# Performance work log

Measured on AMD Instinct MI355X. Metric: run time of the kernel, lower is better.

## Reference

```python
import jax, jax.numpy as jnp
import numpy as np

N = 10000
E = 320000
IN_DIM = 256
HID = 128
HEADS = 3
NEG_SLOPE = 0.2
EPS = 1e-8


def setup_inputs() -> dict:
    key = jax.random.key(0)
    ks = jax.random.split(key, 12)
    rn = lambda k, s, sc=0.1: jax.random.normal(k, s, dtype=jnp.float32) * sc
    return {
        'x1': jax.random.normal(ks[0], (N, IN_DIM), dtype=jnp.float32),
        'edge_index1': jax.random.randint(ks[1], (2, E), 0, N, dtype=jnp.int64),
        'x2': jax.random.normal(ks[2], (N, IN_DIM), dtype=jnp.float32),
        'edge_index2': jax.random.randint(ks[3], (2, E), 0, N, dtype=jnp.int64),
        'W1': rn(ks[4], (IN_DIM, HEADS * HID)),
        'att_src1': rn(ks[5], (HEADS, HID)),
        'att_dst1': rn(ks[6], (HEADS, HID)),
        'b1': rn(ks[7], (HEADS * HID,)),
        'W2': rn(ks[8], (HEADS * HID, HID)),
        'att_src2': rn(ks[9], (1, HID)),
        'att_dst2': rn(ks[10], (1, HID)),
        'b2': rn(ks[11], (HID,)),
    }


def gat_conv(x, edge_index, W, a_src, a_dst, bias, heads, out_ch, concat):
    """PyG-style GATConv with add_self_loops=True."""
    n = x.shape[0]
    loops = jnp.arange(n, dtype=edge_index.dtype)
    ei = jnp.concatenate([edge_index, jnp.stack([loops, loops])], axis=1)
    src, dst = ei[0], ei[1]
    h = (x @ W).reshape(n, heads, out_ch)                    # [N,H,C]
    s = jnp.einsum('nhc,hc->nh', h, a_src)                    # alpha_src per node
    d = jnp.einsum('nhc,hc->nh', h, a_dst)                    # alpha_dst per node
    e = jax.nn.leaky_relu(s[src] + d[dst], NEG_SLOPE)         # [Etot,H]
    m = jax.ops.segment_max(e, dst, num_segments=n)           # segment softmax (stable)
    ex = jnp.exp(e - m[dst])
    denom = jax.ops.segment_sum(ex, dst, num_segments=n)
    alpha = ex / denom[dst]                                   # [Etot,H]
    out = jax.ops.segment_sum(h[src] * alpha[:, :, None], dst, num_segments=n)
    out = out.reshape(n, heads * out_ch) if concat else out.mean(axis=1)
    return out + bias, (ei, alpha)


def _branch(x, ei, W1, as1, ad1, b1, W2, as2, ad2, b2):
    e1, (ei_sl, alpha1) = gat_conv(x, ei, W1, as1, ad1, b1, HEADS, HID, True)
    e1 = jax.nn.relu(e1)
    e2, _ = gat_conv(e1, ei, W2, as2, ad2, b2, 1, HID, False)
    # _graph_pooling
    attn_val = alpha1.mean(axis=1)                            # [Etot]
    node_attn = jax.ops.segment_sum(attn_val, ei_sl[1], num_segments=x.shape[0])
    weighted = e2 * node_attn[:, None]
    pooled = jnp.concatenate([weighted.mean(axis=0), e2.mean(axis=0)])  # [2*HID]
    return pooled, alpha1


def reference(x1, edge_index1, x2, edge_index2, W1, att_src1, att_dst1, b1,
              W2, att_src2, att_dst2, b2):
    g1, alpha1 = _branch(x1, edge_index1, W1, att_src1, att_dst1, b1,
                         W2, att_src2, att_dst2, b2)
    g2, alpha2 = _branch(x2, edge_index2, W1, att_src1, att_dst1, b1,
                         W2, att_src2, att_dst2, b2)
    n1 = jnp.maximum(jnp.linalg.norm(g1), EPS)
    n2 = jnp.maximum(jnp.linalg.norm(g2), EPS)
    sim = jnp.dot(g1, g2) / (n1 * n2)
    return sim, alpha1, alpha2
```

## Files before the change

### kernel.cpp

```cpp
#include <hip/hip_runtime.h>
#include <hip/hip_bf16.h>
#include <cstdint>
#include <cstddef>

#define INDIM 256
#define NEG 0.2f

typedef __attribute__((ext_vector_type(8))) short short8v;
typedef __attribute__((ext_vector_type(4))) float f32x4;
typedef __attribute__((ext_vector_type(2))) float f32x2;

__device__ __forceinline__ unsigned short f2bf(float x) {
  __hip_bfloat16 b = __float2bfloat16(x);
  return __builtin_bit_cast(unsigned short, b);
}

__device__ __forceinline__ unsigned char f2fp8(float v) {
  int packed = __builtin_amdgcn_cvt_pk_fp8_f32(v, v, 0, false);
  return (unsigned char)(packed & 0xff);
}

__device__ __forceinline__ float lrelu(float v) { return v > 0.f ? v : NEG * v; }

__global__ void wprep_kernel(const float* __restrict__ W1, __hip_bfloat16* __restrict__ W1t,
                             const float* __restrict__ W2, __hip_bfloat16* __restrict__ W2t,
                             const float* __restrict__ x1, const float* __restrict__ x2,
                             unsigned short* __restrict__ xb, int N) {
  int idx = blockIdx.x * blockDim.x + threadIdx.x;
  const int T1 = 256 * 384;
  const int T2 = 384 * 128;
  if (idx < T1) {
    int k = idx / 384, c = idx - k * 384;
    W1t[(size_t)c * 256 + k] = __float2bfloat16(W1[idx]);
  } else if (idx < T1 + T2) {
    int i = idx - T1;
    int k = i / 128, c = i - k * 128;
    W2t[(size_t)c * 384 + k] = __float2bfloat16(W2[i]);
  } else {
    int j = idx - T1 - T2;
    if (j < 2 * N * 64) {
      int row = j >> 6, q = j & 63;
      const float* src = (row < N) ? (x1 + (size_t)row * 256) : (x2 + (size_t)(row - N) * 256);
      float4 v = *reinterpret_cast<const float4*>(src + 4 * q);
      uint2 st;
      st.x = (unsigned int)f2bf(v.x) | ((unsigned int)f2bf(v.y) << 16);
      st.y = (unsigned int)f2bf(v.z) | ((unsigned int)f2bf(v.w) << 16);
      *reinterpret_cast<uint2*>(xb + (size_t)row * 256 + 4 * q) = st;
    }
  }
}

template<int K, int SST>
__device__ __forceinline__ void gemm_body(int bx, int by,
                                          const short* __restrict__ Ab,
                                          const __hip_bfloat16* __restrict__ Wt,
                                          const float* __restrict__ att_s,
                                          const float* __restrict__ att_d,
                                          unsigned char* __restrict__ Yc,
                                          float* __restrict__ So,
                                          float* __restrict__ Do,
                                          int M, int NC,
                                          short (*As)[40], short (*Bs)[40],
                                          float (*sred)[64]) {
  const int tid = threadIdx.x;
  const int row0 = bx * 64;
  const int col0 = by * 128;
  const int l = tid & 63, w = tid >> 6;
  const int wr = w >> 1, wc = w & 1;
  const int lr = l & 15, lk = (l >> 4) * 8;

  f32x4 acc[2][4];
#pragma unroll
  for (int m = 0; m < 2; ++m)
#pragma unroll
    for (int n = 0; n < 4; ++n) acc[m][n] = {0.f, 0.f, 0.f, 0.f};

  for (int k0 = 0; k0 < K; k0 += 32) {
    __syncthreads();
    {
      int r = tid >> 2, kq = (tid & 3) * 8;
      int gr = row0 + r;
      short8v av = {0, 0, 0, 0, 0, 0, 0, 0};
      if (gr < M) av = *(const short8v*)(Ab + (size_t)gr * K + k0 + kq);
      *(short8v*)&As[r][kq] = av;
    }
    {
      int c = tid >> 1, kq = (tid & 1) * 8;
      const short* wp = (const short*)Wt + (size_t)(col0 + c) * K + k0 + kq;
      *(short8v*)&Bs[c][kq]      = *(const short8v*)wp;
      *(short8v*)&Bs[c][kq + 16] = *(const short8v*)(wp + 16);
    }
    __syncthreads();
    short8v a[2], b[4];
#pragma unroll
    for (int m = 0; m < 2; ++m) a[m] = *(short8v*)&As[wr * 32 + m * 16 + lr][lk];
#pragma unroll
    for (int n = 0; n < 4; ++n) b[n] = *(short8v*)&Bs[wc * 64 + n * 16 + lr][lk];
#pragma unroll
    for (int m = 0; m < 2; ++m)
#pragma unroll
      for (int n = 0; n < 4; ++n)
        acc[m][n] = __builtin_amdgcn_mfma_f32_16x16x32_bf16(a[m], b[n], acc[m][n], 0, 0, 0);
  }
#pragma unroll
  for (int m = 0; m < 2; ++m) {
    int rbase = row0 + wr * 32 + m * 16 + (l >> 4) * 4;
#pragma unroll
    for (int n = 0; n < 4; ++n) {
      int col = col0 + wc * 64 + n * 16 + lr;
#pragma unroll
      for (int q = 0; q < 4; ++q) {
        int row = rbase + q;
        if (row < M) Yc[(size_t)row * NC + col] = f2fp8(acc[m][n][q]);
      }
    }
  }
  float asv[4], adv[4];
#pragma unroll
  for (int n = 0; n < 4; ++n) {
    int col = col0 + wc * 64 + n * 16 + lr;
    asv[n] = att_s[col];
    adv[n] = att_d[col];
  }
  float ps[2][4], pd[2][4];
#pragma unroll
  for (int m = 0; m < 2; ++m)
#pragma unroll
    for (int q = 0; q < 4; ++q) {
      float s = 0.f, d = 0.f;
#pragma unroll
      for (int n = 0; n < 4; ++n) {
        s = fmaf(acc[m][n][q], asv[n], s);
        d = fmaf(acc[m][n][q], adv[n], d);
      }
      ps[m][q] = s; pd[m][q] = d;
    }
#pragma unroll
  for (int o = 1; o < 16; o <<= 1) {
#pragma unroll
    for (int m = 0; m < 2; ++m)
#pragma unroll
      for (int q = 0; q < 4; ++q) {
        ps[m][q] += __shfl_xor(ps[m][q], o);
        pd[m][q] += __shfl_xor(pd[m][q], o);
      }
  }
  __syncthreads();
  if (wc == 1 && lr == 0) {
#pragma unroll
    for (int m = 0; m < 2; ++m)
#pragma unroll
      for (int q = 0; q < 4; ++q) {
        int rl = wr * 32 + m * 16 + (l >> 4) * 4 + q;
        sred[0][rl] = ps[m][q];
        sred[1][rl] = pd[m][q];
      }
  }
  __syncthreads();
  if (wc == 0 && lr == 0) {
#pragma unroll
    for (int m = 0; m < 2; ++m)
#pragma unroll
      for (int q = 0; q < 4; ++q) {
        int rl = wr * 32 + m * 16 + (l >> 4) * 4 + q;
        int row = row0 + rl;
        if (row < M) {
          So[(size_t)row * SST + by] = ps[m][q] + sred[0][rl];
          Do[(size_t)row * SST + by] = pd[m][q] + sred[1][rl];
        }
      }
  }
}

__global__ __launch_bounds__(256) void gemm1_deg_kernel(const short* __restrict__ xb,
                                                        const __hip_bfloat16* __restrict__ Wt,
                                                        const float* __restrict__ att_s,
                                                        const float* __restrict__ att_d,
                                                        unsigned char* __restrict__ Yc,
                                                        float* __restrict__ So,
                                                        float* __restrict__ Do,
                                                        int M, int gmx,
                                                        const int* __restrict__ ed1,
                                                        const int* __restrict__ ed2,
                                                        int E, int Etot, int N,
                                                        int* __restrict__ deg) {
  __shared__ short As[64][40];
  __shared__ short Bs[128][40];
  __shared__ float sred[2][64];
  int bid = blockIdx.x;
  if (bid < gmx * 3) {
    gemm_body<256, 4>(bid % gmx, bid / gmx, xb, Wt, att_s, att_d,
                      Yc, So, Do, M, 384, As, Bs, sred);
  } else {
    int idx = (bid - gmx * 3) * 256 + threadIdx.x;
    if (idx < 2 * Etot) {
      int br = idx >= Etot;
      int el = idx - br * Etot;
      const int* ed = br ? ed2 : ed1;
      int dn = ((el < E) ? ed[el] : (el - E)) + br * N;
      atomicAdd(&deg[dn], 1);
    }
  }
}

__global__ __launch_bounds__(256) void gemm2_alpha_kernel(const short* __restrict__ e1b,
                                                          const __hip_bfloat16* __restrict__ Wt,
                                                          const float* __restrict__ att_s,
                                                          const float* __restrict__ att_d,
                                                          unsigned char* __restrict__ Yc,
                                                          float* __restrict__ So,
                                                          float* __restrict__ Do,
                                                          int M, int gmx,
                                                          const float* __restrict__ S4,
                                                          const float* __restrict__ D4,
                                                          const float* __restrict__ invden,
                                                          const int* __restrict__ es1,
                                                          const int* __restrict__ ed1,
                                                          const int* __restrict__ es2,
                                                          const int* __restrict__ ed2,
                                                          int E, int Etot, int N,
                                                          float* __restrict__ out) {
  __shared__ short As[64][40];
  __shared__ short Bs[128][40];
  __shared__ float sred[2][64];
  int bid = blockIdx.x;
  if (bid < gmx) {
    gemm_body<384, 1>(bid, 0, e1b, Wt, att_s, att_d,
                      Yc, So, Do, M, 128, As, Bs, sred);
  } else {
    int idx = (bid - gmx) * 256 + threadIdx.x;
    if (idx < 2 * Etot) {
      int br = idx >= Etot;
      int el = idx - br * Etot;
      const int* es = br ? es2 : es1;
      const int* ed = br ? ed2 : ed1;
      int sn, dn;
      if (el < E) { sn = es[el]; dn = ed[el]; } else { sn = dn = el - E; }
      sn += br * N; dn += br * N;
      float* ao = out + 1 + (size_t)br * Etot * 3 + (size_t)el * 3;
#pragma unroll
      for (int h = 0; h < 3; ++h) {
        float v = lrelu(S4[sn * 4 + h] + D4[dn * 4 + h]);
        ao[h] = __expf(v) * invden[dn * 3 + h];
      }
    }
  }
}

__global__ __launch_bounds__(1024) void scan_kernel(const int* __restrict__ deg,
                                                    int* __restrict__ rowptr,
                                                    int* __restrict__ cursor, int n) {
  __shared__ int wsum[16];
  int t = threadIdx.x, lane = t & 63, wid = t >> 6;
  int start = t * 20;
  int v[20];
  int s = 0;
#pragma unroll
  for (int k = 0; k < 20; ++k) {
    int i = start + k;
    int d = (i < n) ? deg[i] : 0;
    s += d;
    v[k] = s;
  }
  int x = s;
#pragma unroll
  for (int o = 1; o < 64; o <<= 1) {
    int tm = __shfl_up(x, o);
    if (lane >= o) x += tm;
  }
  if (lane == 63) wsum[wid] = x;
  __syncthreads();
  if (wid == 0) {
    int wv = (lane < 16) ? wsum[lane] : 0;
#pragma unroll
    for (int o = 1; o < 16; o <<= 1) {
      int tm = __shfl_up(wv, o);
      if (lane >= o) wv += tm;
    }
    if (lane < 16) wsum[lane] = wv;
  }
  __syncthreads();
  int excl = (x - s) + (wid ? wsum[wid - 1] : 0);
  if (t == 0) rowptr[0] = 0;
#pragma unroll
  for (int k = 0; k < 20; ++k) {
    int i = start + k;
    if (i < n) {
      rowptr[i + 1] = excl + v[k];
      cursor[i] = excl + (k ? v[k - 1] : 0);
    }
  }
}

__global__ void fill_kernel(const int* __restrict__ es1, const int* __restrict__ ed1,
                            const int* __restrict__ es2, const int* __restrict__ ed2,
                            int E, int Etot, int N, int* __restrict__ cursor,
                            int* __restrict__ csr_src) {
  int idx = blockIdx.x * blockDim.x + threadIdx.x;
  if (idx >= 2 * Etot) return;
  int br = idx >= Etot;
  int el = idx - br * Etot;
  const int* es = br ? es2 : es1;
  const int* ed = br ? ed2 : ed1;
  int sn, dn;
  if (el < E) { sn = es[el]; dn = ed[el]; } else { sn = dn = el - E; }
  sn += br * N; dn += br * N;
  int pos = atomicAdd(&cursor[dn], 1);
  csr_src[pos] = sn;
}

__global__ __launch_bounds__(256) void agg1_kernel(const unsigned char* __restrict__ h1c,
                                                   const float* __restrict__ S4,
                                                   const float* __restrict__ D4,
                                                   const int* __restrict__ rowptr,
                                                   const int* __restrict__ csr_src,
                                                   const float* __restrict__ b1,
                                                   __hip_bfloat16* __restrict__ e1b,
                                                   float* __restrict__ invden, int N2) {
  __shared__ float4 st[4][64];
  int wv = threadIdx.x >> 6;
  int n = blockIdx.x * 4 + wv;
  if (n >= N2) return;
  int l = threadIdx.x & 63;
  int head = l >> 5;
  const float4* S4v = reinterpret_cast<const float4*>(S4);
  int p0 = rowptr[n], p1 = rowptr[n + 1];
  float d0 = D4[n * 4], d1 = D4[n * 4 + 1], d2 = D4[n * 4 + 2];

  float dp0 = 0.f, dp1 = 0.f, dp2 = 0.f;
  float acc[6] = {0.f, 0.f, 0.f, 0.f, 0.f, 0.f};
  for (int base = p0; base < p1; base += 64) {
    int cnt = min(64, p1 - base);
    if (l < cnt) {
      int sn = csr_src[base + l];
      float4 sv = S4v[sn];
      float e0 = __expf(lrelu(sv.x + d0));
      float e1 = __expf(lrelu(sv.y + d1));
      float e2 = __expf(lrelu(sv.z + d2));
      st[wv][l] = make_float4(__int_as_float(sn), e0, e1, e2);
      dp0 += e0; dp1 += e1; dp2 += e2;
    }
    int i = 0;
    for (; i + 4 <= cnt; i += 4) {
      float4 w[4];
      unsigned int hv[4];
      unsigned short gv[4];
#pragma unroll
      for (int u = 0; u < 4; ++u) {
        w[u] = st[wv][i + u];
        int sn = __float_as_int(w[u].x);
        const unsigned char* row = h1c + (size_t)sn * 384;
        hv[u] = *reinterpret_cast<const unsigned int*>(row + 4 * l);
        gv[u] = *reinterpret_cast<const unsigned short*>(row + 256 + 2 * l);
      }
#pragma unroll
      for (int u = 0; u < 4; ++u) {
        float alo = head ? w[u].z : w[u].y;
        float ahi = w[u].w;
        f32x2 f0 = __builtin_amdgcn_cvt_pk_f32_fp8((int)hv[u], false);
        f32x2 f1 = __builtin_amdgcn_cvt_pk_f32_fp8((int)hv[u], true);
        f32x2 g0 = __builtin_amdgcn_cvt_pk_f32_fp8((int)(unsigned int)gv[u], false);
        acc[0] = fmaf(alo, f0.x, acc[0]);
        acc[1] = fmaf(alo, f0.y, acc[1]);
        acc[2] = fmaf(alo, f1.x, acc[2]);
        acc[3] = fmaf(alo, f1.y, acc[3]);
        acc[4] = fmaf(ahi, g0.x, acc[4]);
        acc[5] = fmaf(ahi, g0.y, acc[5]);
      }
    }
    for (; i < cnt; ++i) {
      float4 w = st[wv][i];
      int sn = __float_as_int(w.x);
      const unsigned char* row = h1c + (size_t)sn * 384;
      unsigned int hv = *reinterpret_cast<const unsigned int*>(row + 4 * l);
      unsigned short gv = *reinterpret_cast<const unsigned short*>(row + 256 + 2 * l);
      float alo = head ? w.z : w.y;
      float ahi = w.w;
      f32x2 f0 = __builtin_amdgcn_cvt_pk_f32_fp8((int)hv, false);
      f32x2 f1 = __builtin_amdgcn_cvt_pk_f32_fp8((int)hv, true);
      f32x2 g0 = __builtin_amdgcn_cvt_pk_f32_fp8((int)(unsigned int)gv, false);
      acc[0] = fmaf(alo, f0.x, acc[0]);
      acc[1] = fmaf(alo, f0.y, acc[1]);
      acc[2] = fmaf(alo, f1.x, acc[2]);
      acc[3] = fmaf(alo, f1.y, acc[3]);
      acc[4] = fmaf(ahi, g0.x, acc[4]);
      acc[5] = fmaf(ahi, g0.y, acc[5]);
    }
  }
#pragma unroll
  for (int o = 32; o; o >>= 1) {
    dp0 += __shfl_down(dp0, o); dp1 += __shfl_down(dp1, o); dp2 += __shfl_down(dp2, o);
  }
  float inv0 = 1.f / __shfl(dp0, 0);
  float inv1 = 1.f / __shfl(dp1, 0);
  float inv2 = 1.f / __shfl(dp2, 0);

  float ilo = head ? inv1 : inv0;
  int c0 = 4 * l;
  float4 bb = *reinterpret_cast<const float4*>(b1 + c0);
  float v0 = acc[0] * ilo + bb.x;
  float v1 = acc[1] * ilo + bb.y;
  float v2 = acc[2] * ilo + bb.z;
  float v3 = acc[3] * ilo + bb.w;
  v0 = v0 > 0.f ? v0 : 0.f; v1 = v1 > 0.f ? v1 : 0.f;
  v2 = v2 > 0.f ? v2 : 0.f; v3 = v3 > 0.f ? v3 : 0.f;
  int ch = 256 + 2 * l;
  float2 bh = *reinterpret_cast<const float2*>(b1 + ch);
  float v4 = acc[4] * inv2 + bh.x;
  float v5 = acc[5] * inv2 + bh.y;
  v4 = v4 > 0.f ? v4 : 0.f; v5 = v5 > 0.f ? v5 : 0.f;
  unsigned short* eb = reinterpret_cast<unsigned short*>(e1b) + (size_t)n * 384;
  uint2 lo;
  lo.x = (unsigned int)f2bf(v0) | ((unsigned int)f2bf(v1) << 16);
  lo.y = (unsigned int)f2bf(v2) | ((unsigned int)f2bf(v3) << 16);
  *reinterpret_cast<uint2*>(eb + c0) = lo;
  *reinterpret_cast<unsigned int*>(eb + ch) =
      (unsigned int)f2bf(v4) | ((unsigned int)f2bf(v5) << 16);
  if (l == 0) invden[n * 3] = inv0;
  else if (l == 1) invden[n * 3 + 1] = inv1;
  else if (l == 2) invden[n * 3 + 2] = inv2;
}

__global__ __launch_bounds__(256) void agg2_kernel(const unsigned char* __restrict__ h2c,
                                                   const float* __restrict__ S2,
                                                   const float* __restrict__ D2,
                                                   const int* __restrict__ rowptr,
                                                   const int* __restrict__ csr_src,
                                                   const float* __restrict__ b2,
                                                   float* __restrict__ e2out, int N2) {
  __shared__ int lsrc[4][256];
  __shared__ float la[4][256];
  const unsigned int* H4 = reinterpret_cast<const unsigned int*>(h2c);
  int wv = threadIdx.x >> 6;
  int n = blockIdx.x * 4 + wv;
  if (n >= N2) return;
  int lane = threadIdx.x & 63;
  int half = lane >> 5, t = lane & 31;
  int p0 = rowptr[n], p1 = rowptr[n + 1];
  float dnv = D2[n];

  float dpart = 0.f;
  float acc[4] = {0.f, 0.f, 0.f, 0.f};
  for (int base = p0; base < p1; base += 256) {
    int cnt = min(256, p1 - base);
    for (int i = lane; i < cnt; i += 64) {
      int sn = csr_src[base + i];
      lsrc[wv][i] = sn;
      float ex = __expf(lrelu(S2[sn] + dnv));
      la[wv][i] = ex;
      dpart += ex;
    }
    int i = half;
    for (; i + 14 < cnt; i += 16) {
      unsigned int hv[8];
      float av[8];
#pragma unroll
      for (int u = 0; u < 8; ++u) {
        int e = i + 2 * u;
        int sn = lsrc[wv][e];
        av[u] = la[wv][e];
        hv[u] = H4[(size_t)sn * 32 + t];
      }
#pragma unroll
      for (int u = 0; u < 8; ++u) {
        f32x2 f0 = __builtin_amdgcn_cvt_pk_f32_fp8((int)hv[u], false);
        f32x2 f1 = __builtin_amdgcn_cvt_pk_f32_fp8((int)hv[u], true);
        acc[0] = fmaf(av[u], f0.x, acc[0]);
        acc[1] = fmaf(av[u], f0.y, acc[1]);
        acc[2] = fmaf(av[u], f1.x, acc[2]);
        acc[3] = fmaf(av[u], f1.y, acc[3]);
      }
    }
    for (; i < cnt; i += 2) {
      int sn = lsrc[wv][i];
      float a = la[wv][i];
      unsigned int hv = H4[(size_t)sn * 32 + t];
      f32x2 f0 = __builtin_amdgcn_cvt_pk_f32_fp8((int)hv, false);
      f32x2 f1 = __builtin_amdgcn_cvt_pk_f32_fp8((int)hv, true);
      acc[0] = fmaf(a, f0.x, acc[0]);
      acc[1] = fmaf(a, f0.y, acc[1]);
      acc[2] = fmaf(a, f1.x, acc[2]);
      acc[3] = fmaf(a, f1.y, acc[3]);
    }
  }
#pragma unroll
  for (int k = 0; k < 4; ++k) acc[k] += __shfl_xor(acc[k], 32);
#pragma unroll
  for (int o = 32; o; o >>= 1) dpart += __shfl_down(dpart, o);
  float invden = 1.f / __shfl(dpart, 0);
  if (half == 0) {
    float4 bb = *reinterpret_cast<const float4*>(b2 + 4 * t);
    float4 ov;
    ov.x = acc[0] * invden + bb.x;
    ov.y = acc[1] * invden + bb.y;
    ov.z = acc[2] * invden + bb.z;
    ov.w = acc[3] * invden + bb.w;
    *reinterpret_cast<float4*>(e2out + (size_t)n * 128 + 4 * t) = ov;
  }
}

__global__ __launch_bounds__(128) void pool_sim_kernel(const float* __restrict__ e2,
                                                       float* __restrict__ g,
                                                       int* __restrict__ cnt,
                                                       int N, float invN,
                                                       float* __restrict__ out) {
  int c = threadIdx.x;
  int br = blockIdx.y;
  int r0 = br * N + blockIdx.x * 128;
  int r1 = min(r0 + 128, br * N + N);
  float acc = 0.f;
  for (int n = r0; n < r1; ++n) acc += e2[(size_t)n * 128 + c];
  atomicAdd(&g[br * 128 + c], acc * invN);
  __threadfence();
  __shared__ bool last;
  __shared__ float sd[128], s1[128], s2[128];
  if (c == 0) {
    int total = gridDim.x * gridDim.y;
    last = (atomicAdd(cnt, 1) == total - 1);
  }
  __syncthreads();
  if (!last) return;
  float a = atomicAdd(&g[c], 0.f);
  float b = atomicAdd(&g[128 + c], 0.f);
  sd[c] = a * b; s1[c] = a * a; s2[c] = b * b;
  __syncthreads();
  for (int ofs = 64; ofs; ofs >>= 1) {
    if (c < ofs) { sd[c] += sd[c + ofs]; s1[c] += s1[c + ofs]; s2[c] += s2[c + ofs]; }
    __syncthreads();
  }
  if (c == 0) {
    float n1 = fmaxf(sqrtf(s1[0]), 1e-8f);
    float n2 = fmaxf(sqrtf(s2[0]), 1e-8f);
    out[0] = sd[0] / (n1 * n2);
  }
}

extern "C" void kernel_launch(void* const* d_in, const int* in_sizes, int n_in,
                              void* d_out, int out_size, void* d_ws, size_t ws_size,
                              hipStream_t stream) {
  const int N = in_sizes[0] / INDIM;
  const int E = in_sizes[1] / 2;
  const int Etot = E + N;
  const int N2 = 2 * N;

  const float* x1  = (const float*)d_in[0];
  const int*   ei1 = (const int*)d_in[1];
  const float* x2  = (const float*)d_in[2];
  const int*   ei2 = (const int*)d_in[3];
  const float* W1  = (const float*)d_in[4];
  const float* as1 = (const float*)d_in[5];
  const float* ad1 = (const float*)d_in[6];
  const float* b1  = (const float*)d_in[7];
  const float* W2  = (const float*)d_in[8];
  const float* as2 = (const float*)d_in[9];
  const float* ad2 = (const float*)d_in[10];
  const float* b2  = (const float*)d_in[11];
  float* out = (float*)d_out;
  const int* es1 = ei1, *ed1 = ei1 + E;
  const int* es2 = ei2, *ed2 = ei2 + E;

  char* p = (char*)d_ws;
  auto alloc = [&](size_t bytes) -> char* {
    char* q = p;
    p += (bytes + 255) & ~(size_t)255;
    return q;
  };
  float* g   = (float*)alloc(256 * 4);
  int*   cnt = (int*)alloc(256);
  int*   deg = (int*)alloc((size_t)N2 * 4);
  size_t zero_bytes = (size_t)((char*)deg - (char*)g) + (((size_t)N2 * 4 + 255) & ~(size_t)255);

  unsigned short* xb = (unsigned short*)alloc((size_t)N2 * 256 * 2);
  unsigned char* h1c = (unsigned char*)alloc((size_t)N2 * 384);
  __hip_bfloat16* e1b = (__hip_bfloat16*)alloc((size_t)N2 * 384 * 2);
  unsigned char* h2c = (unsigned char*)alloc((size_t)N2 * 128);
  float* e2          = (float*)alloc((size_t)N2 * 128 * 4);
  __hip_bfloat16* W1t = (__hip_bfloat16*)alloc((size_t)256 * 384 * 2);
  __hip_bfloat16* W2t = (__hip_bfloat16*)alloc((size_t)384 * 128 * 2);
  float* s1v  = (float*)alloc((size_t)N2 * 4 * 4);
  float* d1v  = (float*)alloc((size_t)N2 * 4 * 4);
  float* s2v  = (float*)alloc((size_t)N2 * 4);
  float* d2v  = (float*)alloc((size_t)N2 * 4);
  float* idn  = (float*)alloc((size_t)N2 * 3 * 4);
  int* rowptr  = (int*)alloc((size_t)(N2 + 1) * 4);
  int* cursor  = (int*)alloc((size_t)N2 * 4);
  int* csr_src = (int*)alloc((size_t)2 * Etot * 4);

  const int EB = 256;
  const int egrid2 = (2 * Etot + EB - 1) / EB;
  const int gmx = (N2 + 63) / 64;
  const int wtot = 256 * 384 + 384 * 128 + N2 * 64;

  hipMemsetAsync(g, 0, zero_bytes, stream);
  wprep_kernel<<<(wtot + 255) / 256, 256, 0, stream>>>(W1, W1t, W2, W2t, x1, x2, xb, N);

  gemm1_deg_kernel<<<gmx * 3 + egrid2, 256, 0, stream>>>((const short*)xb, W1t, as1, ad1,
                                                         h1c, s1v, d1v, N2, gmx,
                                                         ed1, ed2, E, Etot, N, deg);
  scan_kernel<<<1, 1024, 0, stream>>>(deg, rowptr, cursor, N2);
  fill_kernel<<<egrid2, EB, 0, stream>>>(es1, ed1, es2, ed2, E, Etot, N, cursor, csr_src);

  agg1_kernel<<<(N2 + 3) / 4, 256, 0, stream>>>(h1c, s1v, d1v, rowptr, csr_src, b1,
                                                e1b, idn, N2);

  gemm2_alpha_kernel<<<gmx + egrid2, 256, 0, stream>>>((const short*)e1b, W2t, as2, ad2,
                                                       h2c, s2v, d2v, N2, gmx,
                                                       s1v, d1v, idn,
                                                       es1, ed1, es2, ed2, E, Etot, N, out);
  agg2_kernel<<<(N2 + 3) / 4, 256, 0, stream>>>(h2c, s2v, d2v, rowptr, csr_src, b2, e2, N2);

  pool_sim_kernel<<<dim3((N + 127) / 128, 2), 128, 0, stream>>>(e2, g, cnt, N,
                                                                1.f / (float)N, out);
}
```

Before: 224.6 us.

## Load GEMM MFMA operands directly from global memory with register prefetch

Removes the shared-memory staging of A and B tiles and the two per-iteration barriers in the GEMM body. Each lane now loads its MFMA fragments straight from global memory into registers, prefetches the next k-slice while the current MFMAs run, and the k-loop is fully unrolled. This trades LDS traffic and synchronisation for redundant global or L2 loads, since several waves fetch the same rows and columns, and for higher register pressure. Out-of-range rows are clamped to row 0 rather than zero-filled, so they compute garbage that the existing row<M guard on stores is expected to discard.

```diff
diff --git a/kernel.cpp b/kernel.cpp
--- a/kernel.cpp
+++ b/kernel.cpp
@@ -21,6 +21,10 @@
 }
 
 __device__ __forceinline__ float lrelu(float v) { return v > 0.f ? v : NEG * v; }
+
+__device__ __forceinline__ short8v ld16(const short* p) {
+  return *reinterpret_cast<const short8v*>(p);
+}
 
 __global__ void wprep_kernel(const float* __restrict__ W1, __hip_bfloat16* __restrict__ W1t,
                              const float* __restrict__ W2, __hip_bfloat16* __restrict__ W2t,
@@ -53,14 +57,13 @@
 template<int K, int SST>
 __device__ __forceinline__ void gemm_body(int bx, int by,
                                           const short* __restrict__ Ab,
-                                          const __hip_bfloat16* __restrict__ Wt,
+                                          const short* __restrict__ Wt,
                                           const float* __restrict__ att_s,
                                           const float* __restrict__ att_d,
                                           unsigned char* __restrict__ Yc,
                                           float* __restrict__ So,
                                           float* __restrict__ Do,
                                           int M, int NC,
-                                          short (*As)[40], short (*Bs)[40],
                                           float (*sred)[64]) {
   const int tid = threadIdx.x;
   const int row0 = bx * 64;
@@ -69,38 +72,40 @@
   const int wr = w >> 1, wc = w & 1;
   const int lr = l & 15, lk = (l >> 4) * 8;
 
+  int r0a = row0 + wr * 32 + lr;
+  int r1a = r0a + 16;
+  const short* pa0 = Ab + (size_t)(r0a < M ? r0a : 0) * K + lk;
+  const short* pa1 = Ab + (size_t)(r1a < M ? r1a : 0) * K + lk;
+  const short* pb[4];
+#pragma unroll
+  for (int n = 0; n < 4; ++n)
+    pb[n] = Wt + (size_t)(col0 + wc * 64 + n * 16 + lr) * K + lk;
+
   f32x4 acc[2][4];
 #pragma unroll
   for (int m = 0; m < 2; ++m)
 #pragma unroll
     for (int n = 0; n < 4; ++n) acc[m][n] = {0.f, 0.f, 0.f, 0.f};
 
+  short8v a0 = ld16(pa0), a1 = ld16(pa1);
+  short8v b0 = ld16(pb[0]), b1 = ld16(pb[1]), b2 = ld16(pb[2]), b3 = ld16(pb[3]);
+#pragma unroll
   for (int k0 = 0; k0 < K; k0 += 32) {
-    __syncthreads();
-    {
-      int r = tid >> 2, kq = (tid & 3) * 8;
-      int gr = row0 + r;
-      short8v av = {0, 0, 0, 0, 0, 0, 0, 0};
-      if (gr < M) av = *(const short8v*)(Ab + (size_t)gr * K + k0 + kq);
-      *(short8v*)&As[r][kq] = av;
-    }
-    {
-      int c = tid >> 1, kq = (tid & 1) * 8;
-      const short* wp = (const short*)Wt + (size_t)(col0 + c) * K + k0 + kq;
-      *(short8v*)&Bs[c][kq]      = *(const short8v*)wp;
-      *(short8v*)&Bs[c][kq + 16] = *(const short8v*)(wp + 16);
-    }
-    __syncthreads();
-    short8v a[2], b[4];
-#pragma unroll
-    for (int m = 0; m < 2; ++m) a[m] = *(short8v*)&As[wr * 32 + m * 16 + lr][lk];
-#pragma unroll
-    for (int n = 0; n < 4; ++n) b[n] = *(short8v*)&Bs[wc * 64 + n * 16 + lr][lk];
-#pragma unroll
-    for (int m = 0; m < 2; ++m)
-#pragma unroll
-      for (int n = 0; n < 4; ++n)
-        acc[m][n] = __builtin_amdgcn_mfma_f32_16x16x32_bf16(a[m], b[n], acc[m][n], 0, 0, 0);
+    short8v na0, na1, nb0, nb1, nb2, nb3;
+    if (k0 + 32 < K) {
+      na0 = ld16(pa0 + k0 + 32); na1 = ld16(pa1 + k0 + 32);
+      nb0 = ld16(pb[0] + k0 + 32); nb1 = ld16(pb[1] + k0 + 32);
+      nb2 = ld16(pb[2] + k0 + 32); nb3 = ld16(pb[3] + k0 + 32);
+    }
+    acc[0][0] = __builtin_amdgcn_mfma_f32_16x16x32_bf16(a0, b0, acc[0][0], 0, 0, 0);
+    acc[1][0] = __builtin_amdgcn_mfma_f32_16x16x32_bf16(a1, b0, acc[1][0], 0, 0, 0);
+    acc[0][1] = __builtin_amdgcn_mfma_f32_16x16x32_bf16(a0, b1, acc[0][1], 0, 0, 0);
+    acc[1][1] = __builtin_amdgcn_mfma_f32_16x16x32_bf16(a1, b1, acc[1][1], 0, 0, 0);
+    acc[0][2] = __builtin_amdgcn_mfma_f32_16x16x32_bf16(a0, b2, acc[0][2], 0, 0, 0);
+    acc[1][2] = __builtin_amdgcn_mfma_f32_16x16x32_bf16(a1, b2, acc[1][2], 0, 0, 0);
+    acc[0][3] = __builtin_amdgcn_mfma_f32_16x16x32_bf16(a0, b3, acc[0][3], 0, 0, 0);
+    acc[1][3] = __builtin_amdgcn_mfma_f32_16x16x32_bf16(a1, b3, acc[1][3], 0, 0, 0);
+    a0 = na0; a1 = na1; b0 = nb0; b1 = nb1; b2 = nb2; b3 = nb3;
   }
 #pragma unroll
   for (int m = 0; m < 2; ++m) {
@@ -184,13 +189,11 @@
                                                         const int* __restrict__ ed2,
                                                         int E, int Etot, int N,
                                                         int* __restrict__ deg) {
-  __shared__ short As[64][40];
-  __shared__ short Bs[128][40];
   __shared__ float sred[2][64];
   int bid = blockIdx.x;
   if (bid < gmx * 3) {
-    gemm_body<256, 4>(bid % gmx, bid / gmx, xb, Wt, att_s, att_d,
-                      Yc, So, Do, M, 384, As, Bs, sred);
+    gemm_body<256, 4>(bid % gmx, bid / gmx, xb, (const short*)Wt, att_s, att_d,
+                      Yc, So, Do, M, 384, sred);
   } else {
     int idx = (bid - gmx * 3) * 256 + threadIdx.x;
     if (idx < 2 * Etot) {
@@ -220,13 +223,11 @@
                                                           const int* __restrict__ ed2,
                                                           int E, int Etot, int N,
                                                           float* __restrict__ out) {
-  __shared__ short As[64][40];
-  __shared__ short Bs[128][40];
   __shared__ float sred[2][64];
   int bid = blockIdx.x;
   if (bid < gmx) {
-    gemm_body<384, 1>(bid, 0, e1b, Wt, att_s, att_d,
-                      Yc, So, Do, M, 128, As, Bs, sred);
+    gemm_body<384, 1>(bid, 0, e1b, (const short*)Wt, att_s, att_d,
+                      Yc, So, Do, M, 128, sred);
   } else {
     int idx = (bid - gmx) * 256 + threadIdx.x;
     if (idx < 2 * Etot) {
```

After: 242.2 us. +7.9%, slower.
